# Performance work log

Hardware: AMD Instinct MI355X
Metric: run time of the kernel (lower is better)

## Reference

```python
import jax, jax.numpy as jnp
import numpy as np

B, N_PER, DEG, F_IN, F_HID = 64, 1024, 16, 128, 128
E = B * N_PER * DEG  # 1,048,576 edges, grouped per graph


def setup_inputs() -> dict:
    key = jax.random.key(0)
    ks = jax.random.split(key, 16)
    n_total = B * N_PER
    x = jax.random.normal(ks[0], (n_total, F_IN), dtype=jnp.float32)
    # edges are random within each graph block
    local = jax.random.randint(ks[1], (2, E), 0, N_PER)
    offs = (jnp.arange(E, dtype=jnp.int64) // (N_PER * DEG)) * N_PER
    edge_index = (local.astype(jnp.int64) + offs[None, :])
    edge_weight = jax.random.uniform(ks[2], (E,), dtype=jnp.float32)
    batch_index = jnp.repeat(jnp.arange(B, dtype=jnp.int64), N_PER)
    s = 1.0 / np.sqrt(F_HID)
    params = {
        'W1': jax.random.normal(ks[3], (F_IN, F_HID)) * s,
        'b1': jnp.zeros((F_HID,), jnp.float32),
        'p1': jax.random.normal(ks[4], (F_HID,)) * s,
        'W2': jax.random.normal(ks[5], (F_HID, F_HID)) * s,
        'b2': jnp.zeros((F_HID,), jnp.float32),
        'p2': jax.random.normal(ks[6], (F_HID,)) * s,
        'W3': jax.random.normal(ks[7], (F_HID, F_HID)) * s,
        'b3': jnp.zeros((F_HID,), jnp.float32),
        'p3': jax.random.normal(ks[8], (F_HID,)) * s,
        'Wo': jax.random.normal(ks[9], (2 * F_HID, 1)) * s,
        'bo': jnp.zeros((1,), jnp.float32),
    }
    return {'x': x, 'edge_index': edge_index, 'edge_weight': edge_weight,
            'batch_index': batch_index, **params}


def _gcn_conv(x, src, dst, w, W, b):
    # GCNConv with add_self_loops=True, symmetric normalization, edge_weight.
    n = x.shape[0]
    xW = x @ W
    deg = jnp.zeros((n,), x.dtype).at[dst].add(w) + 1.0  # +1 from self-loop fill
    dinv = jax.lax.rsqrt(deg)
    norm = dinv[src] * w * dinv[dst]
    agg = jnp.zeros_like(xW).at[dst].add(norm[:, None] * xW[src])
    return agg + (dinv * dinv)[:, None] * xW + b  # self-loop term + bias


def _topk_pool(x, src, dst, w, p, n, k):
    # TopKPooling with nonlinearity=sigmoid, equal-size graphs (n -> k nodes).
    f = x.shape[1]
    xr = x.reshape(B, n, f)
    score = jax.nn.sigmoid((xr @ p) / jnp.linalg.norm(p))  # [B, n]
    vals, perm = jax.lax.top_k(score, k)                    # per-graph top-k
    xn = jnp.take_along_axis(xr, perm[:, :, None], axis=1) * vals[:, :, None]
    # inverse map old local idx -> new local idx (-1 if dropped)
    inv = jnp.full((B, n), -1, dtype=jnp.int32)
    inv = inv.at[jnp.arange(B)[:, None], perm].set(jnp.arange(k, dtype=jnp.int32)[None, :])
    g = src // n
    sl = inv[g, src % n]
    dl = inv[dst // n, dst % n]
    keep = (sl >= 0) & (dl >= 0)
    # dropped edges are masked to node 0 with weight 0 (contribute nothing)
    src2 = jnp.where(keep, g * k + sl, 0)
    dst2 = jnp.where(keep, (dst // n) * k + dl, 0)
    w2 = jnp.where(keep, w, jnp.zeros((), w.dtype))
    return xn.reshape(B * k, f), src2, dst2, w2


def reference(x, edge_index, edge_weight, batch_index,
              W1, b1, p1, W2, b2, p2, W3, b3, p3, Wo, bo):
    src, dst = edge_index[0], edge_index[1]
    w = edge_weight
    n = N_PER
    h = _gcn_conv(x, src, dst, w, W1, b1)
    h, src, dst, w = _topk_pool(h, src, dst, w, p1, n, n // 2); n //= 2
    h = jax.nn.relu(h)
    h = _gcn_conv(h, src, dst, w, W2, b2)
    h, src, dst, w = _topk_pool(h, src, dst, w, p2, n, n // 2); n //= 2
    h = jax.nn.relu(h)
    h = _gcn_conv(h, src, dst, w, W3, b3)
    h, src, dst, w = _topk_pool(h, src, dst, w, p3, n, n // 2); n //= 2
    h = jax.nn.relu(h)
    hr = h.reshape(B, n, -1)
    cat = jnp.concatenate([hr.max(axis=1), hr.mean(axis=1)], axis=1)  # gmp || gap
    out = jax.nn.sigmoid(cat @ Wo + bo)
    return out, cat
```

## Files before the change

kernel.cpp:

```cpp
#include <hip/hip_runtime.h>

#define NB 64
#define EDGES 1048576
#define NTOT  65536

struct __align__(8) CsrE { int s; float w; };

using bf16x8 = __attribute__((ext_vector_type(8))) short;
using f32x4  = __attribute__((ext_vector_type(4))) float;

__global__ void k_zerof(float* __restrict__ p, int n){
  int i=blockIdx.x*256+threadIdx.x; if(i<n) p[i]=0.f;
}

__device__ inline void split1(float x, unsigned &hi16, unsigned &lo16){
  unsigned b=__float_as_uint(x);
  unsigned h=(b+0x7FFFu+((b>>16)&1u))&0xFFFF0000u;
  float lf=x-__uint_as_float(h);
  unsigned lb=__float_as_uint(lf);
  hi16=h>>16;
  lo16=(lb+0x7FFFu+((lb>>16)&1u))>>16;
}

__device__ inline void split8(const float4&u, const float4&v, bf16x8&hi, bf16x8&lo){
  float e[8]={u.x,u.y,u.z,u.w,v.x,v.y,v.z,v.w};
  #pragma unroll
  for(int j=0;j<8;++j){
    unsigned h16,l16; split1(e[j],h16,l16);
    hi[j]=(short)h16; lo[j]=(short)l16;
  }
}

__global__ __launch_bounds__(256) void k_wpack(const float* __restrict__ W1,
        const float* __restrict__ W2, const float* __restrict__ W3,
        unsigned* __restrict__ outp){
  int b=blockIdx.x, m=b>>3;
  const float* W = (m==0)?W1:((m==1)?W2:W3);
  unsigned* o = outp + m*16384;
  for(int t=(b&7)*256+threadIdx.x; t<8192; t+=2048){
    int i=t&3, l=(t>>2)&63, c=(t>>8)&7, q=(t>>11)&3;
    int col=c*16+(l&15);
    int k0=q*32+((l>>4)<<3)+i*2;
    float x0=W[k0*128+col], x1=W[(k0+1)*128+col];
    unsigned h0,l0,h1,l1;
    split1(x0,h0,l0); split1(x1,h1,l1);
    int base=((q*8+c)*2)*256;
    o[base + l*4 + i]       = (h1<<16)|h0;
    o[base + 256 + l*4 + i] = (l1<<16)|l0;
  }
}

template<bool G, int S>
__global__ __launch_bounds__(256) void mm_mfma(const float* __restrict__ X,
        const unsigned* __restrict__ Wpk, const int* __restrict__ selold,
        const float* __restrict__ score, float* __restrict__ Y, int gshift){
  __shared__ __align__(16) unsigned Wl[16384];
  const int RPB = 64*S;
  int b=blockIdx.x;
  int row0b;
  if(G){
    int xcd=b&7, slot=b>>3, bpg=1<<gshift;
    int graph=xcd*8+(slot>>gshift), idx=slot&(bpg-1);
    row0b = graph*(bpg*RPB) + idx*RPB;
  } else row0b = b*RPB;
  for(int t=threadIdx.x;t<4096;t+=256)
    ((uint4*)Wl)[t]=((const uint4*)Wpk)[t];
  const int wave=threadIdx.x>>6, lane=threadIdx.x&63;
  const int row0 = row0b + wave*(16*S);
  const int lrow=lane&15, lko=(lane>>4)<<3;
  int orow[S]; float scr[S];
  #pragma unroll
  for(int s=0;s<S;++s){
    int rr=row0+s*16+lrow;
    orow[s]=G?selold[rr]:rr;
    scr[s]=G?score[orow[s]]:1.f;
  }
  const f32x4 vzero={0.f,0.f,0.f,0.f};
  f32x4 acc[S][8];
  #pragma unroll
  for(int s=0;s<S;++s){
    #pragma unroll
    for(int c=0;c<8;++c) acc[s][c]=vzero;
  }
  __syncthreads();
  const char* wb=(const char*)Wl + lane*16;
  float4 u[S],v[S];
  #pragma unroll
  for(int s=0;s<S;++s){
    const float* xp=X+(size_t)orow[s]*128+lko;
    u[s]=*(const float4*)xp; v[s]=*(const float4*)(xp+4);
  }
  #pragma unroll
  for(int q=0;q<4;++q){
    float4 un[S],vn[S];
    if(q<3){
      #pragma unroll
      for(int s=0;s<S;++s){
        const float* xp=X+(size_t)orow[s]*128+(q+1)*32+lko;
        un[s]=*(const float4*)xp; vn[s]=*(const float4*)(xp+4);
      }
    }
    bf16x8 Ah[S],Al[S];
    #pragma unroll
    for(int s=0;s<S;++s){
      if(G){
        u[s].x=fmaxf(u[s].x*scr[s],0.f); u[s].y=fmaxf(u[s].y*scr[s],0.f);
        u[s].z=fmaxf(u[s].z*scr[s],0.f); u[s].w=fmaxf(u[s].w*scr[s],0.f);
        v[s].x=fmaxf(v[s].x*scr[s],0.f); v[s].y=fmaxf(v[s].y*scr[s],0.f);
        v[s].z=fmaxf(v[s].z*scr[s],0.f); v[s].w=fmaxf(v[s].w*scr[s],0.f);
      }
      split8(u[s],v[s],Ah[s],Al[s]);
    }
    #pragma unroll
    for(int c=0;c<8;++c){
      const bf16x8 bh=*(const bf16x8*)(wb + (q*8+c)*2048);
      const bf16x8 bl=*(const bf16x8*)(wb + (q*8+c)*2048 + 1024);
      #pragma unroll
      for(int s=0;s<S;++s){
        acc[s][c]=__builtin_amdgcn_mfma_f32_16x16x32_bf16(Ah[s],bh,acc[s][c],0,0,0);
        acc[s][c]=__builtin_amdgcn_mfma_f32_16x16x32_bf16(Al[s],bh,acc[s][c],0,0,0);
        acc[s][c]=__builtin_amdgcn_mfma_f32_16x16x32_bf16(Ah[s],bl,acc[s][c],0,0,0);
      }
    }
    if(q<3){
      #pragma unroll
      for(int s=0;s<S;++s){ u[s]=un[s]; v[s]=vn[s]; }
    }
  }
  const int dcol=lane&15, dr0=(lane>>4)<<2;
  #pragma unroll
  for(int s=0;s<S;++s){
    #pragma unroll
    for(int c=0;c<8;++c){
      #pragma unroll
      for(int r=0;r<4;++r){
        Y[(size_t)(row0+s*16+dr0+r)*128 + c*16 + dcol]=acc[s][c][r];
      }
    }
  }
}

__global__ __launch_bounds__(1024) void k_count(const int* __restrict__ edst,
        const float* __restrict__ ew, int* __restrict__ chunkcnt, float* __restrict__ chunkw){
  __shared__ int lc[1024];
  __shared__ float lw[1024];
  int b=blockIdx.x, i=threadIdx.x;
  int xcd=b&7, slot=b>>3;
  int graph=xcd*8+(slot&7), chunk=slot>>3;
  int e0=graph*16384+chunk*4096;
  lc[i]=0; lw[i]=0.f;
  __syncthreads();
  for(int e=e0+i; e<e0+4096; e+=1024){
    int dl=edst[e]&1023;
    atomicAdd(&lc[dl],1);
    atomicAdd(&lw[dl],ew[e]);
  }
  __syncthreads();
  chunkcnt[chunk*65536+graph*1024+i]=lc[i];
  chunkw  [chunk*65536+graph*1024+i]=lw[i];
}

__global__ __launch_bounds__(1024) void k_scan_graph(const int* __restrict__ chunkcnt,
        const float* __restrict__ chunkw, int* __restrict__ rowptr,
        float* __restrict__ dinv1, int* __restrict__ fill){
  __shared__ int pre[1024];
  int g=blockIdx.x, i=threadIdx.x;
  int o=g*1024+i;
  int c = chunkcnt[o]+chunkcnt[65536+o]+chunkcnt[131072+o]+chunkcnt[196608+o];
  float wsum = chunkw[o]+chunkw[65536+o]+chunkw[131072+o]+chunkw[196608+o];
  pre[i]=c; __syncthreads();
  for(int off=1;off<1024;off<<=1){
    int t=(i>=off)?pre[i-off]:0; __syncthreads();
    pre[i]+=t; __syncthreads();
  }
  int excl=pre[i]-c;
  int e0=g*16384;
  rowptr[o]=e0+excl;
  fill[o]=e0+excl;
  dinv1[o]=rsqrtf(wsum+1.0f);
  if(g==63 && i==1023) rowptr[65536]=EDGES;
}

__global__ __launch_bounds__(1024) void k_scatter2(const int* __restrict__ esrc,
        const int* __restrict__ edst, const float* __restrict__ ew,
        int* __restrict__ fill, CsrE* __restrict__ csr){
  int b=blockIdx.x, i=threadIdx.x;
  int xcd=b&7, slot=b>>3;
  int graph=xcd*8+(slot&7), chunk=slot>>3;
  int e0=graph*16384+chunk*4096;
  int base=graph*1024;
  for(int e=e0+i; e<e0+4096; e+=1024){
    int dl=edst[e]&1023;
    int pos=atomicAdd(&fill[base+dl],1);
    CsrE ce; ce.s=esrc[e]; ce.w=ew[e];
    csr[pos]=ce;
  }
}

template<bool F>
__global__ __launch_bounds__(256) void k_gather(const float* __restrict__ xw, const CsrE* __restrict__ csr,
        const int* __restrict__ rowptr, const int* __restrict__ map, const int* __restrict__ inv,
        const float* __restrict__ dinvv, const float* __restrict__ bias, const float* __restrict__ p,
        float* __restrict__ h, float* __restrict__ score, int gshift, int ns){
  int wv=threadIdx.x>>6, half=(threadIdx.x>>5)&1, hl=threadIdx.x&31;
  int b=blockIdx.x, xcd=b&7, slot=b>>3, bpg=1<<gshift;
  int graph=xcd*8+(slot>>gshift), idx=slot&(bpg-1);
  int v = graph*(bpg<<3) + (idx<<3) + wv*2 + half;
  if(v>=ns) return;
  int d0 = F? map[v] : v;
  float dv=dinvv[v];
  int rs=rowptr[d0], re=rowptr[d0+1];
  const int f4=hl*4;
  float4 accA={0.f,0.f,0.f,0.f}, accB={0.f,0.f,0.f,0.f};
  for(int base=rs; base<re; base+=32){
    int len=re-base; if(len>32) len=32;
    int sidx=0; float cf=0.f;
    if(hl<len){
      CsrE en=csr[base+hl];
      int s=en.s; bool live=true;
      if(F){ int t=inv[s]; live=(t>=0); s=live?t:0; }
      if(live){ sidx=s; cf=dinvv[s]*en.w; }
    }
    int len4=(len+3)&~3;
    for(int j=0;j<len4;j+=4){
      float c0=__shfl(cf,j,32),   c1=__shfl(cf,j+1,32);
      float c2=__shfl(cf,j+2,32), c3=__shfl(cf,j+3,32);
      int   s0=__shfl(sidx,j,32),   s1=__shfl(sidx,j+1,32);
      int   s2=__shfl(sidx,j+2,32), s3=__shfl(sidx,j+3,32);
      const float4 x0=*(const float4*)&xw[(size_t)s0*128+f4];
      const float4 x1=*(const float4*)&xw[(size_t)s1*128+f4];
      const float4 x2=*(const float4*)&xw[(size_t)s2*128+f4];
      const float4 x3=*(const float4*)&xw[(size_t)s3*128+f4];
      accA.x+=c0*x0.x; accA.y+=c0*x0.y; accA.z+=c0*x0.z; accA.w+=c0*x0.w;
      accB.x+=c1*x1.x; accB.y+=c1*x1.y; accB.z+=c1*x1.z; accB.w+=c1*x1.w;
      accA.x+=c2*x2.x; accA.y+=c2*x2.y; accA.z+=c2*x2.z; accA.w+=c2*x2.w;
      accB.x+=c3*x3.x; accB.y+=c3*x3.y; accB.z+=c3*x3.z; accB.w+=c3*x3.w;
    }
  }
  float4 acc; acc.x=accA.x+accB.x; acc.y=accA.y+accB.y;
  acc.z=accA.z+accB.z; acc.w=accA.w+accB.w;
  const float4 xv=*(const float4*)&xw[(size_t)v*128+f4];
  const float4 bv=*(const float4*)&bias[f4];
  float d2=dv*dv;
  float4 hv;
  hv.x=acc.x*dv + d2*xv.x + bv.x;
  hv.y=acc.y*dv + d2*xv.y + bv.y;
  hv.z=acc.z*dv + d2*xv.z + bv.z;
  hv.w=acc.w*dv + d2*xv.w + bv.w;
  *(float4*)&h[(size_t)v*128+f4]=hv;
  const float4 pv=*(const float4*)&p[f4];
  float z=hv.x*pv.x+hv.y*pv.y+hv.z*pv.z+hv.w*pv.w;
  float pp=pv.x*pv.x+pv.y*pv.y+pv.z*pv.z+pv.w*pv.w;
  #pragma unroll
  for(int m=16;m>0;m>>=1){ z+=__shfl_xor(z,m,32); pp+=__shfl_xor(pp,m,32); }
  if(hl==0) score[v]=1.0f/(1.0f+expf(-z/sqrtf(pp)));
}

template<int N, int K, int MODE>
__global__ __launch_bounds__(1024) void k_topk(const float* __restrict__ score,
        int* __restrict__ inv, int* __restrict__ selold,
        const int* __restrict__ inv1s, const int* __restrict__ sel1s,
        int* __restrict__ inv12, int* __restrict__ map12,
        const int* __restrict__ rowptr, const CsrE* __restrict__ csr,
        float* __restrict__ dinv_out){
  __shared__ unsigned hist[256];
  __shared__ unsigned sfx[256];
  __shared__ int c_sh, r_sh;
  __shared__ int pre[N];
  int g=blockIdx.x, i=threadIdx.x;
  int gv=g*N+i;
  unsigned key=__float_as_uint(score[gv]);
  int st=1;
  if(i==0) r_sh=K;
  __syncthreads();
  int R=K;
  #pragma unroll
  for(int pass=0; pass<4; ++pass){
    int shift=24-pass*8;
    if(i<256) hist[i]=0;
    __syncthreads();
    unsigned byte=(key>>shift)&255u;
    if(st==1) atomicAdd(&hist[byte],1u);
    __syncthreads();
    if(i<256) sfx[i]=hist[i];
    __syncthreads();
    for(int off=1; off<256; off<<=1){
      unsigned t=0;
      if(i<256 && i+off<256) t=sfx[i+off];
      __syncthreads();
      if(i<256) sfx[i]+=t;
      __syncthreads();
    }
    if(i<256){
      int A=(i<255)?(int)sfx[i+1]:0;
      if(A<R && R<=A+(int)hist[i]){ c_sh=i; r_sh=R-A; }
    }
    __syncthreads();
    int c=c_sh; R=r_sh;
    if(st==1){
      if((int)byte>c) st=2;
      else if((int)byte<c) st=0;
    }
    __syncthreads();
  }
  int alive=(st==1)?1:0;
  pre[i]=alive; __syncthreads();
  for(int off=1;off<N;off<<=1){
    int t=(i>=off)?pre[i-off]:0; __syncthreads();
    pre[i]+=t; __syncthreads();
  }
  int tie_rank=pre[i]-alive;
  int sel=(st==2)||(st==1 && tie_rank<R);
  __syncthreads();
  pre[i]=sel; __syncthreads();
  for(int off=1;off<N;off<<=1){
    int t=(i>=off)?pre[i-off]:0; __syncthreads();
    pre[i]+=t; __syncthreads();
  }
  int ng=g*K+pre[i]-1;
  if(sel && ng<NB*K){ inv[gv]=ng; selold[ng]=gv; }
  else inv[gv]=-1;
  if(MODE==1){
    __syncthreads();
    for(int t=i; t<K; t+=N){
      int v=g*K+t;
      int d0=selold[v];
      int rs=rowptr[d0], re=rowptr[d0+1];
      float s0=0.f,s1=0.f,s2=0.f,s3=0.f;
      int e=rs;
      for(; e+4<=re; e+=4){
        CsrE e0=csr[e], e1=csr[e+1], e2=csr[e+2], e3=csr[e+3];
        if(inv[e0.s]>=0) s0+=e0.w;
        if(inv[e1.s]>=0) s1+=e1.w;
        if(inv[e2.s]>=0) s2+=e2.w;
        if(inv[e3.s]>=0) s3+=e3.w;
      }
      for(; e<re; ++e){
        CsrE en=csr[e];
        if(inv[en.s]>=0) s0+=en.w;
      }
      dinv_out[v]=rsqrtf((s0+s1)+(s2+s3)+1.0f);
    }
  }
  if(MODE==2){
    __syncthreads();
    for(int t=i; t<1024; t+=N){
      int v0=g*1024+t;
      int q=inv1s[v0];
      inv12[v0]=(q>=0)?inv[q]:-1;
    }
    for(int t=i; t<K; t+=N){
      int v=g*K+t;
      map12[v]=sel1s[selold[v]];
    }
    __syncthreads();
    for(int t=i; t<K; t+=N){
      int v=g*K+t;
      int d0=map12[v];
      int rs=rowptr[d0], re=rowptr[d0+1];
      float s0=0.f,s1=0.f,s2=0.f,s3=0.f;
      int e=rs;
      for(; e+4<=re; e+=4){
        CsrE e0=csr[e], e1=csr[e+1], e2=csr[e+2], e3=csr[e+3];
        if(inv12[e0.s]>=0) s0+=e0.w;
        if(inv12[e1.s]>=0) s1+=e1.w;
        if(inv12[e2.s]>=0) s2+=e2.w;
        if(inv12[e3.s]>=0) s3+=e3.w;
      }
      for(; e<re; ++e){
        CsrE en=csr[e];
        if(inv12[en.s]>=0) s0+=en.w;
      }
      dinv_out[v]=rsqrtf((s0+s1)+(s2+s3)+1.0f);
    }
  }
}

__global__ __launch_bounds__(128) void k_readout(const float* __restrict__ h3, const float* __restrict__ score3,
                                                 const int* __restrict__ selold3,
                                                 const float* __restrict__ Wo, const float* __restrict__ bo,
                                                 float* __restrict__ out){
  __shared__ float red[128];
  int g=blockIdx.x, f=threadIdx.x;
  float mx=-3.4e38f, sm=0.f;
  for(int nd=0;nd<128;++nd){
    int old=selold3[g*128+nd];
    float v=fmaxf(h3[(size_t)old*128+f]*score3[old],0.f);
    mx=fmaxf(mx,v); sm+=v;
  }
  float mean=sm*(1.0f/128.0f);
  out[64+g*256+f]    =mx;
  out[64+g*256+128+f]=mean;
  red[f]=mx*Wo[f]+mean*Wo[128+f];
  __syncthreads();
  for(int off=64;off>0;off>>=1){ if(f<off) red[f]+=red[f+off]; __syncthreads(); }
  if(f==0){ float z=red[0]+bo[0]; out[g]=1.0f/(1.0f+expf(-z)); }
}

extern "C" void kernel_launch(void* const* d_in, const int* in_sizes, int n_in,
                              void* d_out, int out_size, void* d_ws, size_t ws_size,
                              hipStream_t stream) {
  (void)in_sizes; (void)n_in;
  const float* x  = (const float*)d_in[0];
  const int*   ei = (const int*)d_in[1];
  const float* ew = (const float*)d_in[2];
  const float* W1=(const float*)d_in[4];  const float* b1=(const float*)d_in[5];  const float* p1=(const float*)d_in[6];
  const float* W2=(const float*)d_in[7];  const float* b2=(const float*)d_in[8];  const float* p2=(const float*)d_in[9];
  const float* W3=(const float*)d_in[10]; const float* b3=(const float*)d_in[11]; const float* p3=(const float*)d_in[12];
  const float* Wo=(const float*)d_in[13]; const float* bo=(const float*)d_in[14];
  float* out=(float*)d_out;

  char* ws=(char*)d_ws;
  size_t cur=0;
  float* slot0=(float*)(ws+cur); cur+=33554432;
  float* slot1=(float*)(ws+cur); cur+=33554432;
  CsrE*  csr  =(CsrE*)(ws+cur);  cur+=(size_t)EDGES*8;
  int*   chunkcnt=(int*)(ws+cur); cur+=1048576;
  float* chunkw  =(float*)(ws+cur); cur+=1048576;
  int*   fill =(int*)  (ws+cur); cur+=262144;
  int*   rowptr=(int*) (ws+cur); cur+=262400;
  float* dinv1=(float*)(ws+cur); cur+=262144;
  float* dinv2=(float*)(ws+cur); cur+=131072;
  float* dinv3=(float*)(ws+cur); cur+=65536;
  float* sc1  =(float*)(ws+cur); cur+=262144;
  float* sc2  =(float*)(ws+cur); cur+=131072;
  float* sc3  =(float*)(ws+cur); cur+=65536;
  int*   inv1 =(int*)  (ws+cur); cur+=262144;
  int*   inv2 =(int*)  (ws+cur); cur+=131072;
  int*   invS =(int*)  (ws+cur); cur+=65536;
  int*   inv12=(int*)  (ws+cur); cur+=262144;
  int*   sel1 =(int*)  (ws+cur); cur+=131072;
  int*   sel2 =(int*)  (ws+cur); cur+=65536;
  int*   sel3 =(int*)  (ws+cur); cur+=32768;
  int*   map12=(int*)  (ws+cur); cur+=65536;
  unsigned* wpk=(unsigned*)(ws+cur); cur+=196608;

  if (ws_size < cur) {
    k_zerof<<<(out_size+255)/256,256,0,stream>>>(out,out_size);
    return;
  }

  const int* esrc=ei; const int* edst=ei+EDGES;

  k_wpack<<<24,256,0,stream>>>(W1,W2,W3,wpk);

  mm_mfma<false,2><<<NTOT/128,256,0,stream>>>(x,wpk,nullptr,nullptr,slot0,0);
  k_count<<<256,1024,0,stream>>>(edst,ew,chunkcnt,chunkw);
  k_scan_graph<<<64,1024,0,stream>>>(chunkcnt,chunkw,rowptr,dinv1,fill);
  k_scatter2<<<256,1024,0,stream>>>(esrc,edst,ew,fill,csr);
  k_gather<false><<<NTOT/8,256,0,stream>>>(slot0,csr,rowptr,nullptr,nullptr,
                                           dinv1,b1,p1,slot1,sc1,7,NTOT);
  k_topk<1024,512,1><<<NB,1024,0,stream>>>(sc1,inv1,sel1,nullptr,nullptr,nullptr,nullptr,
                                           rowptr,csr,dinv2);

  mm_mfma<true,1><<<32768/64,256,0,stream>>>(slot1,wpk+16384,sel1,sc1,slot0,3);
  k_gather<true><<<32768/8,256,0,stream>>>(slot0,csr,rowptr,sel1,inv1,
                                           dinv2,b2,p2,slot1,sc2,6,32768);
  k_topk<512,256,2><<<NB,512,0,stream>>>(sc2,inv2,sel2,inv1,sel1,inv12,map12,
                                         rowptr,csr,dinv3);

  mm_mfma<true,1><<<16384/64,256,0,stream>>>(slot1,wpk+32768,sel2,sc2,slot0,2);
  k_gather<true><<<16384/8,256,0,stream>>>(slot0,csr,rowptr,map12,inv12,
                                           dinv3,b3,p3,slot1,sc3,5,16384);
  k_topk<256,128,0><<<NB,256,0,stream>>>(sc3,invS,sel3,nullptr,nullptr,nullptr,nullptr,
                                         nullptr,nullptr,nullptr);

  k_readout<<<NB,128,0,stream>>>(slot1,sc3,sel3,Wo,bo,out);
}
```

Measured before the change: 312.1 us.

## Replace shared-memory Hillis-Steele scans with wavefront shuffles/ballots and fuse readout into top-k

The block-wide prefix scans in the graph scan and top-k kernels are rewritten with 64-lane wavefront shuffle scans and ballot/popcount ranks plus a small per-wave total array. This replaces dozens of __syncthreads barriers per scan with a few. The readout kernel is merged into the last top-k launch as MODE 3, removing one kernel launch. Launch bounds now match the block size N. The cost is a serial loop over wave totals and more template complexity.

```diff
diff --git a/kernel.cpp b/kernel.cpp
--- a/kernel.cpp
+++ b/kernel.cpp
@@ -163,21 +163,24 @@
 __global__ __launch_bounds__(1024) void k_scan_graph(const int* __restrict__ chunkcnt,
         const float* __restrict__ chunkw, int* __restrict__ rowptr,
         float* __restrict__ dinv1, int* __restrict__ fill){
-  __shared__ int pre[1024];
+  __shared__ int wsum[16];
   int g=blockIdx.x, i=threadIdx.x;
+  int lane=i&63, w=i>>6;
   int o=g*1024+i;
   int c = chunkcnt[o]+chunkcnt[65536+o]+chunkcnt[131072+o]+chunkcnt[196608+o];
-  float wsum = chunkw[o]+chunkw[65536+o]+chunkw[131072+o]+chunkw[196608+o];
-  pre[i]=c; __syncthreads();
-  for(int off=1;off<1024;off<<=1){
-    int t=(i>=off)?pre[i-off]:0; __syncthreads();
-    pre[i]+=t; __syncthreads();
-  }
-  int excl=pre[i]-c;
+  float ws = chunkw[o]+chunkw[65536+o]+chunkw[131072+o]+chunkw[196608+o];
+  int v=c;
+  #pragma unroll
+  for(int off=1;off<64;off<<=1){ int t=__shfl_up(v,off,64); if(lane>=off) v+=t; }
+  if(lane==63) wsum[w]=v;
+  __syncthreads();
+  int base=0;
+  for(int k=0;k<w;++k) base+=wsum[k];
+  int excl=base+v-c;
   int e0=g*16384;
   rowptr[o]=e0+excl;
   fill[o]=e0+excl;
-  dinv1[o]=rsqrtf(wsum+1.0f);
+  dinv1[o]=rsqrtf(ws+1.0f);
   if(g==63 && i==1023) rowptr[65536]=EDGES;
 }
 
@@ -257,22 +260,23 @@
 }
 
 template<int N, int K, int MODE>
-__global__ __launch_bounds__(1024) void k_topk(const float* __restrict__ score,
+__global__ __launch_bounds__(N) void k_topk(const float* __restrict__ score,
         int* __restrict__ inv, int* __restrict__ selold,
         const int* __restrict__ inv1s, const int* __restrict__ sel1s,
         int* __restrict__ inv12, int* __restrict__ map12,
         const int* __restrict__ rowptr, const CsrE* __restrict__ csr,
-        float* __restrict__ dinv_out){
+        float* __restrict__ dinv_out,
+        const float* __restrict__ h3, const float* __restrict__ Wo,
+        const float* __restrict__ bo, float* __restrict__ outp){
   __shared__ unsigned hist[256];
-  __shared__ unsigned sfx[256];
+  __shared__ int wsum[16];
   __shared__ int c_sh, r_sh;
-  __shared__ int pre[N];
+  __shared__ float red[128];
   int g=blockIdx.x, i=threadIdx.x;
+  int lane=i&63, w=i>>6;
   int gv=g*N+i;
   unsigned key=__float_as_uint(score[gv]);
   int st=1;
-  if(i==0) r_sh=K;
-  __syncthreads();
   int R=K;
   #pragma unroll
   for(int pass=0; pass<4; ++pass){
@@ -282,18 +286,23 @@
     unsigned byte=(key>>shift)&255u;
     if(st==1) atomicAdd(&hist[byte],1u);
     __syncthreads();
-    if(i<256) sfx[i]=hist[i];
-    __syncthreads();
-    for(int off=1; off<256; off<<=1){
-      unsigned t=0;
-      if(i<256 && i+off<256) t=sfx[i+off];
-      __syncthreads();
-      if(i<256) sfx[i]+=t;
-      __syncthreads();
-    }
+    unsigned hcnt=0, sfx=0;
     if(i<256){
-      int A=(i<255)?(int)sfx[i+1]:0;
-      if(A<R && R<=A+(int)hist[i]){ c_sh=i; r_sh=R-A; }
+      hcnt=hist[i]; sfx=hcnt;
+      #pragma unroll
+      for(int off=1;off<64;off<<=1){
+        unsigned t=__shfl_down(sfx,off,64);
+        if(lane+off<64) sfx+=t;
+      }
+      if(lane==0) wsum[w]=(int)sfx;
+    }
+    __syncthreads();
+    if(i<256){
+      int tot=0;
+      for(int k=w+1;k<4;++k) tot+=wsum[k];
+      int S=(int)sfx+tot;
+      int A=S-(int)hcnt;
+      if(A<R && R<=S){ c_sh=i; r_sh=R-A; }
     }
     __syncthreads();
     int c=c_sh; R=r_sh;
@@ -304,20 +313,22 @@
     __syncthreads();
   }
   int alive=(st==1)?1:0;
-  pre[i]=alive; __syncthreads();
-  for(int off=1;off<N;off<<=1){
-    int t=(i>=off)?pre[i-off]:0; __syncthreads();
-    pre[i]+=t; __syncthreads();
-  }
-  int tie_rank=pre[i]-alive;
+  unsigned long long mA=__ballot(alive);
+  int rA=__popcll(mA & ((1ULL<<lane)-1ULL));
+  if(lane==0) wsum[w]=__popcll(mA);
+  __syncthreads();
+  int offA=0;
+  for(int k=0;k<w;++k) offA+=wsum[k];
+  int tie_rank=offA+rA;
   int sel=(st==2)||(st==1 && tie_rank<R);
   __syncthreads();
-  pre[i]=sel; __syncthreads();
-  for(int off=1;off<N;off<<=1){
-    int t=(i>=off)?pre[i-off]:0; __syncthreads();
-    pre[i]+=t; __syncthreads();
-  }
-  int ng=g*K+pre[i]-1;
+  unsigned long long mS=__ballot(sel);
+  int rS=__popcll(mS & ((1ULL<<lane)-1ULL));
+  if(lane==0) wsum[w]=__popcll(mS);
+  __syncthreads();
+  int offS=0;
+  for(int k=0;k<w;++k) offS+=wsum[k];
+  int ng=g*K+offS+rS;
   if(sel && ng<NB*K){ inv[gv]=ng; selold[ng]=gv; }
   else inv[gv]=-1;
   if(MODE==1){
@@ -374,27 +385,28 @@
       dinv_out[v]=rsqrtf((s0+s1)+(s2+s3)+1.0f);
     }
   }
-}
-
-__global__ __launch_bounds__(128) void k_readout(const float* __restrict__ h3, const float* __restrict__ score3,
-                                                 const int* __restrict__ selold3,
-                                                 const float* __restrict__ Wo, const float* __restrict__ bo,
-                                                 float* __restrict__ out){
-  __shared__ float red[128];
-  int g=blockIdx.x, f=threadIdx.x;
-  float mx=-3.4e38f, sm=0.f;
-  for(int nd=0;nd<128;++nd){
-    int old=selold3[g*128+nd];
-    float v=fmaxf(h3[(size_t)old*128+f]*score3[old],0.f);
-    mx=fmaxf(mx,v); sm+=v;
-  }
-  float mean=sm*(1.0f/128.0f);
-  out[64+g*256+f]    =mx;
-  out[64+g*256+128+f]=mean;
-  red[f]=mx*Wo[f]+mean*Wo[128+f];
-  __syncthreads();
-  for(int off=64;off>0;off>>=1){ if(f<off) red[f]+=red[f+off]; __syncthreads(); }
-  if(f==0){ float z=red[0]+bo[0]; out[g]=1.0f/(1.0f+expf(-z)); }
+  if(MODE==3){
+    __syncthreads();
+    int f=i;
+    float mx=-3.4e38f, sm=0.f;
+    if(f<128){
+      for(int nd=0;nd<128;++nd){
+        int old=selold[g*128+nd];
+        float vv=fmaxf(h3[(size_t)old*128+f]*score[old],0.f);
+        mx=fmaxf(mx,vv); sm+=vv;
+      }
+      float mean=sm*(1.0f/128.0f);
+      outp[64+g*256+f]    =mx;
+      outp[64+g*256+128+f]=mean;
+      red[f]=mx*Wo[f]+mean*Wo[128+f];
+    }
+    __syncthreads();
+    for(int off=64;off>0;off>>=1){
+      if(f<off) red[f]+=red[f+off];
+      __syncthreads();
+    }
+    if(f==0){ float z=red[0]+bo[0]; outp[g]=1.0f/(1.0f+expf(-z)); }
+  }
 }
 
 extern "C" void kernel_launch(void* const* d_in, const int* in_sizes, int n_in,
@@ -451,19 +463,17 @@
   k_gather<false><<<NTOT/8,256,0,stream>>>(slot0,csr,rowptr,nullptr,nullptr,
                                            dinv1,b1,p1,slot1,sc1,7,NTOT);
   k_topk<1024,512,1><<<NB,1024,0,stream>>>(sc1,inv1,sel1,nullptr,nullptr,nullptr,nullptr,
-                                           rowptr,csr,dinv2);
+                                           rowptr,csr,dinv2,nullptr,nullptr,nullptr,nullptr);
 
   mm_mfma<true,1><<<32768/64,256,0,stream>>>(slot1,wpk+16384,sel1,sc1,slot0,3);
   k_gather<true><<<32768/8,256,0,stream>>>(slot0,csr,rowptr,sel1,inv1,
                                            dinv2,b2,p2,slot1,sc2,6,32768);
   k_topk<512,256,2><<<NB,512,0,stream>>>(sc2,inv2,sel2,inv1,sel1,inv12,map12,
-                                         rowptr,csr,dinv3);
+                                         rowptr,csr,dinv3,nullptr,nullptr,nullptr,nullptr);
 
   mm_mfma<true,1><<<16384/64,256,0,stream>>>(slot1,wpk+32768,sel2,sc2,slot0,2);
   k_gather<true><<<16384/8,256,0,stream>>>(slot0,csr,rowptr,map12,inv12,
                                            dinv3,b3,p3,slot1,sc3,5,16384);
-  k_topk<256,128,0><<<NB,256,0,stream>>>(sc3,invS,sel3,nullptr,nullptr,nullptr,nullptr,
-                                         nullptr,nullptr,nullptr);
-
-  k_readout<<<NB,128,0,stream>>>(slot1,sc3,sel3,Wo,bo,out);
-}
+  k_topk<256,128,3><<<NB,256,0,stream>>>(sc3,invS,sel3,nullptr,nullptr,nullptr,nullptr,
+                                         nullptr,nullptr,nullptr,slot1,Wo,bo,out);
+}
```

After: 300.0 us. 3.9% less time.
